# Kernel tuning notes

Measured on AMD Instinct MI355X. Metric: run time of the kernel, lower is better.

Reference implementation:

```python
import jax, jax.numpy as jnp
import numpy as np

H = 128
G = 8192            # num session graphs
TOTAL = 409600      # total nodes across all graphs
MAX_ITEM = 10000


def setup_inputs() -> dict:
    key = jax.random.key(0)
    ks = jax.random.split(key, 16)
    rng = np.random.default_rng(0)
    # variable-length sections that sum exactly to TOTAL
    secs = rng.integers(10, 90, size=G - 1)
    last = TOTAL - int(secs.sum())
    assert last >= 1
    sections = np.concatenate([secs, [last]]).astype(np.int32)
    segment_ids = np.repeat(np.arange(G, dtype=np.int32), sections)
    last_idx = (np.cumsum(sections) - 1).astype(np.int32)

    s = 0.02
    inp = {
        "node_embedding": jax.random.normal(ks[0], (TOTAL, H), jnp.float32),
        "num_count": jax.random.uniform(ks[1], (TOTAL,), jnp.float32),
        "sections": jnp.asarray(sections),
        "segment_ids": jnp.asarray(segment_ids),
        "last_idx": jnp.asarray(last_idx),
        "item_embedding_table": jax.random.normal(ks[2], (MAX_ITEM, H), jnp.float32),
        "user_embedding": jax.random.normal(ks[3], (G, H), jnp.float32),
        "u_n_repeat": jnp.zeros((G, H), jnp.float32),
        "max_item_id": MAX_ITEM,
        "W1_w": jax.random.normal(ks[4], (H, H), jnp.float32) * s,
        "W1_b": jnp.zeros((H,), jnp.float32),
        "W2_w": jax.random.normal(ks[5], (H, H), jnp.float32) * s,
        "W2_b": jnp.zeros((H,), jnp.float32),
        "q_w": jax.random.normal(ks[6], (1, H), jnp.float32) * s,
        "q_b": jnp.zeros((1,), jnp.float32),
        "W3_w": jax.random.normal(ks[7], (H, 2 * H), jnp.float32) * s,
        "W3_b": jnp.zeros((H,), jnp.float32),
    }
    return inp


def reference(node_embedding, num_count, sections, segment_ids, last_idx,
              item_embedding_table, user_embedding, u_n_repeat, max_item_id,
              W1_w, W1_b, W2_w, W2_b, q_w, q_b, W3_w, W3_b):
    num_graphs = last_idx.shape[0]
    # last node of each graph, [G, H]
    v_n = node_embedding[last_idx]
    # broadcast last node back to every node of its graph (replaces torch.split repeat loop)
    v_n_rep = v_n[segment_ids]                          # [N, H]
    gate = jax.nn.sigmoid(v_n_rep @ W1_w.T + W1_b + node_embedding @ W2_w.T + W2_b)
    alpha = gate @ q_w.T + q_b                          # [N, 1]
    s_g_whole = num_count[:, None] * alpha * node_embedding  # [N, H]
    s_g = jax.ops.segment_sum(s_g_whole, segment_ids, num_segments=num_graphs)  # [G, H]
    s_h = jnp.concatenate([v_n, s_g], axis=1) @ W3_w.T + W3_b  # [G, H]
    return s_h
```

## Files before the change

### kernel.cpp

```cpp
#include <hip/hip_runtime.h>
#include <hip/hip_bf16.h>

#define H_DIM  128
#define NGRAPH 8192
#define NTOTAL 409600
#define NBLK2  (NTOTAL / 128)

#define NLOG2E -1.4426950408889634f

typedef __attribute__((ext_vector_type(8))) short    s16x8;
typedef __attribute__((ext_vector_type(4))) float    f32x4;
typedef __attribute__((ext_vector_type(4))) unsigned u32x4;

__device__ __forceinline__ unsigned short f2bf(float f) {
    unsigned int u = __float_as_uint(f);
    unsigned int r = u + 0x7fffu + ((u >> 16) & 1u);
    return (unsigned short)(r >> 16);
}

__global__ void k0_w2(const float* __restrict__ W2w, unsigned short* __restrict__ w2bf) {
    int i = blockIdx.x * 256 + threadIdx.x;
    w2bf[i] = f2bf(NLOG2E * W2w[i]);
}

__global__ __launch_bounds__(128) void k1_ag(
    const float* __restrict__ node_emb,
    const int*   __restrict__ last_idx,
    const float* __restrict__ W1w,
    const float* __restrict__ W1b,
    const float* __restrict__ W2b,
    float* __restrict__ a_g,
    float* __restrict__ s_g)
{
    __shared__ float vn[4][H_DIM];
    const int tid = threadIdx.x;
    const int g0  = blockIdx.x * 4;
    #pragma unroll
    for (int g = 0; g < 4; g++) {
        int li = last_idx[g0 + g];
        vn[g][tid] = node_emb[(size_t)li * H_DIM + tid];
        s_g[(size_t)(g0 + g) * H_DIM + tid] = 0.f;
    }
    __syncthreads();
    float b = W1b[tid] + W2b[tid];
    float a0 = b, a1 = b, a2 = b, a3 = b;
    const float* wrow = W1w + (size_t)tid * H_DIM;
    #pragma unroll 8
    for (int k = 0; k < H_DIM; k += 4) {
        float4 w = *reinterpret_cast<const float4*>(wrow + k);
        a0 += w.x * vn[0][k] + w.y * vn[0][k+1] + w.z * vn[0][k+2] + w.w * vn[0][k+3];
        a1 += w.x * vn[1][k] + w.y * vn[1][k+1] + w.z * vn[1][k+2] + w.w * vn[1][k+3];
        a2 += w.x * vn[2][k] + w.y * vn[2][k+1] + w.z * vn[2][k+2] + w.w * vn[2][k+3];
        a3 += w.x * vn[3][k] + w.y * vn[3][k+1] + w.z * vn[3][k+2] + w.w * vn[3][k+3];
    }
    a_g[(size_t)(g0 + 0) * H_DIM + tid] = NLOG2E * a0;
    a_g[(size_t)(g0 + 1) * H_DIM + tid] = NLOG2E * a1;
    a_g[(size_t)(g0 + 2) * H_DIM + tid] = NLOG2E * a2;
    a_g[(size_t)(g0 + 3) * H_DIM + tid] = NLOG2E * a3;
}

__global__ __launch_bounds__(512, 6) void k2_fused(
    const float* __restrict__ node_emb,
    const float* __restrict__ num_count,
    const int*   __restrict__ seg_ids,
    const float* __restrict__ a_g,
    const unsigned short* __restrict__ w2bf,
    const float* __restrict__ q_w,
    const float* __restrict__ q_b,
    float* __restrict__ s_g)
{
    __shared__ __align__(16) char w2s[H_DIM * 256];

    const int tid = threadIdx.x;
    {
        const uint4* wsrc = reinterpret_cast<const uint4*>(w2bf);
        #pragma unroll
        for (int i = 0; i < 4; i++) {
            int c = i * 512 + tid;
            uint4 v = wsrc[c];
            int byte = c << 4;
            int row  = byte >> 8;
            *reinterpret_cast<uint4*>(w2s + (byte ^ ((row & 7) << 4))) = v;
        }
    }

    const int bid = (int)blockIdx.x;
    const int swz = (bid & 7) * (NBLK2 / 8) + (bid >> 3);

    const int lane = tid & 63;
    const int wid  = tid >> 6;
    const int l16 = lane & 15, lq = lane >> 4;
    const int nb  = (swz * 8 + wid) * 16;

    const int   sgl = seg_ids[nb + l16];
    const float ncl = num_count[nb + l16];
    const float qb0 = q_b[0];

    const float* agrow = a_g + (size_t)sgl * H_DIM + lq * 4;
    f32x4 acc[8];
    #pragma unroll
    for (int nt = 0; nt < 8; nt++) {
        float4 a4 = *reinterpret_cast<const float4*>(agrow + nt * 16);
        acc[nt] = f32x4{a4.x, a4.y, a4.z, a4.w};
    }

    s16x8 af[4];
    const float* nrow = node_emb + (size_t)(nb + l16) * H_DIM + lq * 8;
    #pragma unroll
    for (int ks = 0; ks < 4; ks++) {
        float4 f0 = *reinterpret_cast<const float4*>(nrow + ks * 32);
        float4 f1 = *reinterpret_cast<const float4*>(nrow + ks * 32 + 4);
        unsigned p0, p1, p2, p3;
        asm("v_cvt_pk_bf16_f32 %0, %1, %2" : "=v"(p0) : "v"(f0.x), "v"(f0.y));
        asm("v_cvt_pk_bf16_f32 %0, %1, %2" : "=v"(p1) : "v"(f0.z), "v"(f0.w));
        asm("v_cvt_pk_bf16_f32 %0, %1, %2" : "=v"(p2) : "v"(f1.x), "v"(f1.y));
        asm("v_cvt_pk_bf16_f32 %0, %1, %2" : "=v"(p3) : "v"(f1.z), "v"(f1.w));
        union { u32x4 u; s16x8 s; } cv;
        cv.u = u32x4{p0, p1, p2, p3};
        af[ks] = cv.s;
    }

    __syncthreads();

    #pragma unroll
    for (int ks = 0; ks < 4; ks++) {
        #pragma unroll
        for (int nt = 0; nt < 8; nt++) {
            int row  = nt * 16 + l16;
            int byte = (row << 8) | ((lq * 8 + ks * 32) << 1);
            byte ^= (row & 7) << 4;
            s16x8 wfr = *reinterpret_cast<const s16x8*>(w2s + byte);
            acc[nt] = __builtin_amdgcn_mfma_f32_16x16x32_bf16(wfr, af[ks], acc[nt], 0, 0, 0);
        }
    }

    float pp0 = 0.f, pp1 = 0.f, pp2 = 0.f, pp3 = 0.f;
    #pragma unroll
    for (int nt = 0; nt < 8; nt++) {
        float4 q4 = *reinterpret_cast<const float4*>(q_w + nt * 16 + lq * 4);
        pp0 += q4.x * __builtin_amdgcn_rcpf(1.f + __builtin_amdgcn_exp2f(acc[nt][0]));
        pp1 += q4.y * __builtin_amdgcn_rcpf(1.f + __builtin_amdgcn_exp2f(acc[nt][1]));
        pp2 += q4.z * __builtin_amdgcn_rcpf(1.f + __builtin_amdgcn_exp2f(acc[nt][2]));
        pp3 += q4.w * __builtin_amdgcn_rcpf(1.f + __builtin_amdgcn_exp2f(acc[nt][3]));
    }
    float p = (pp0 + pp1) + (pp2 + pp3);
    p += __shfl_xor(p, 16, 64);
    p += __shfl_xor(p, 32, 64);
    const float coefl = ncl * (p + qb0);

    s16x8 ib[2];
    #pragma unroll
    for (int b = 0; b < 2; b++) {
        int kk = l16 + 16 * b;
        #pragma unroll
        for (int e = 0; e < 8; e++)
            ib[b][e] = (kk == lq * 8 + e) ? (short)0x3F80 : (short)0;
    }
    f32x4 accT[4][2];
    #pragma unroll
    for (int ks = 0; ks < 4; ks++)
        #pragma unroll
        for (int b = 0; b < 2; b++)
            accT[ks][b] = __builtin_amdgcn_mfma_f32_16x16x32_bf16(
                              af[ks], ib[b], f32x4{0.f, 0.f, 0.f, 0.f}, 0, 0, 0);

    int r0 = 0;
    while (r0 < 16) {
        const int cur = __shfl(sgl, r0, 64);
        unsigned long long diff = __ballot(sgl != cur) & 0xFFFFull;
        diff &= ~((1ull << r0) - 1ull);
        const int r1 = diff ? (int)__builtin_ctzll(diff) : 16;

        const float cmask = (sgl == cur) ? coefl : 0.f;
        float cm[4];
        #pragma unroll
        for (int rr = 0; rr < 4; rr++)
            cm[rr] = __shfl(cmask, lq * 4 + rr, 64);

        #pragma unroll
        for (int ks = 0; ks < 4; ks++) {
            #pragma unroll
            for (int b = 0; b < 2; b++) {
                float s = cm[0] * accT[ks][b][0] + cm[1] * accT[ks][b][1]
                        + cm[2] * accT[ks][b][2] + cm[3] * accT[ks][b][3];
                s += __shfl_xor(s, 16, 64);
                s += __shfl_xor(s, 32, 64);
                if (lq == 0)
                    atomicAdd(s_g + (size_t)cur * H_DIM + ks * 32 + b * 16 + l16, s);
            }
        }
        r0 = r1;
    }
}

__global__ __launch_bounds__(128) void k3_out(
    const float* __restrict__ node_emb,
    const int*   __restrict__ last_idx,
    const float* __restrict__ s_g,
    const float* __restrict__ W3w,
    const float* __restrict__ W3b,
    float* __restrict__ out)
{
    __shared__ float cat[8][2 * H_DIM];
    const int tid = threadIdx.x;
    const int g0  = blockIdx.x * 8;
    #pragma unroll
    for (int g = 0; g < 8; g++) {
        cat[g][tid]         = node_emb[(size_t)last_idx[g0 + g] * H_DIM + tid];
        cat[g][H_DIM + tid] = s_g[(size_t)(g0 + g) * H_DIM + tid];
    }
    __syncthreads();
    float acc[8];
    float b = W3b[tid];
    #pragma unroll
    for (int g = 0; g < 8; g++) acc[g] = b;
    const float* wrow = W3w + (size_t)tid * (2 * H_DIM);
    for (int k = 0; k < 2 * H_DIM; k += 4) {
        float4 w = *reinterpret_cast<const float4*>(wrow + k);
        #pragma unroll
        for (int g = 0; g < 8; g++)
            acc[g] += w.x * cat[g][k] + w.y * cat[g][k+1]
                    + w.z * cat[g][k+2] + w.w * cat[g][k+3];
    }
    #pragma unroll
    for (int g = 0; g < 8; g++)
        out[(size_t)(g0 + g) * H_DIM + tid] = acc[g];
}

extern "C" void kernel_launch(void* const* d_in, const int* in_sizes, int n_in,
                              void* d_out, int out_size, void* d_ws, size_t ws_size,
                              hipStream_t stream) {
    const float* node_emb  = (const float*)d_in[0];
    const float* num_count = (const float*)d_in[1];
    const int*   seg_ids   = (const int*)d_in[3];
    const int*   last_idx  = (const int*)d_in[4];
    const float* W1w = (const float*)d_in[9];
    const float* W1b = (const float*)d_in[10];
    const float* W2w = (const float*)d_in[11];
    const float* W2b = (const float*)d_in[12];
    const float* qw  = (const float*)d_in[13];
    const float* qb  = (const float*)d_in[14];
    const float* W3w = (const float*)d_in[15];
    const float* W3b = (const float*)d_in[16];
    float* out = (float*)d_out;

    char* ws = (char*)d_ws;
    float* a_g = (float*)(ws);
    float* s_g = (float*)(ws + (4u << 20));
    unsigned short* w2bf = (unsigned short*)(ws + (8u << 20));

    k0_w2   <<<64,         256, 0, stream>>>(W2w, w2bf);
    k1_ag   <<<NGRAPH / 4, 128, 0, stream>>>(node_emb, last_idx, W1w, W1b, W2b, a_g, s_g);
    k2_fused<<<NBLK2,      512, 0, stream>>>(node_emb, num_count, seg_ids, a_g,
                                             w2bf, qw, qb, s_g);
    k3_out  <<<NGRAPH / 8, 128, 0, stream>>>(node_emb, last_idx, s_g, W3w, W3b, out);
}
```

Measured before the change: 107.2 us.

## Reduce segment sums in LDS per block and merge boundary partials in a gather kernel

Global atomicAdd into s_g is replaced by LDS atomics into a per-block table of up to 14 local graphs. After a sync, each block writes interior graphs straight to s_g and writes the partial sums of its first and last boundary graphs to a part buffer. A new gather kernel adds up the partials for graphs that span blocks, so s_g no longer needs zeroing in k1. The occupancy hint rises from 6 to 8 blocks per CU. This trades global atomic traffic for an extra launch, about 7 KB more LDS per block, and the assumption that no 128-node block touches more than 14 graphs.

```diff
diff --git a/kernel.cpp b/kernel.cpp
--- a/kernel.cpp
+++ b/kernel.cpp
@@ -5,6 +5,7 @@
 #define NGRAPH 8192
 #define NTOTAL 409600
 #define NBLK2  (NTOTAL / 128)
+#define MAXLOC 14
 
 #define NLOG2E -1.4426950408889634f
 
@@ -29,8 +30,7 @@
     const float* __restrict__ W1w,
     const float* __restrict__ W1b,
     const float* __restrict__ W2b,
-    float* __restrict__ a_g,
-    float* __restrict__ s_g)
+    float* __restrict__ a_g)
 {
     __shared__ float vn[4][H_DIM];
     const int tid = threadIdx.x;
@@ -39,7 +39,6 @@
     for (int g = 0; g < 4; g++) {
         int li = last_idx[g0 + g];
         vn[g][tid] = node_emb[(size_t)li * H_DIM + tid];
-        s_g[(size_t)(g0 + g) * H_DIM + tid] = 0.f;
     }
     __syncthreads();
     float b = W1b[tid] + W2b[tid];
@@ -59,20 +58,26 @@
     a_g[(size_t)(g0 + 3) * H_DIM + tid] = NLOG2E * a3;
 }
 
-__global__ __launch_bounds__(512, 6) void k2_fused(
+__global__ __launch_bounds__(512, 8) void k2_fused(
     const float* __restrict__ node_emb,
     const float* __restrict__ num_count,
     const int*   __restrict__ seg_ids,
+    const int*   __restrict__ last_idx,
     const float* __restrict__ a_g,
     const unsigned short* __restrict__ w2bf,
     const float* __restrict__ q_w,
     const float* __restrict__ q_b,
-    float* __restrict__ s_g)
+    float* __restrict__ s_g,
+    float* __restrict__ part)
 {
     __shared__ __align__(16) char w2s[H_DIM * 256];
+    __shared__ float ldsS[MAXLOC][H_DIM];
 
     const int tid = threadIdx.x;
     {
+        float* z = &ldsS[0][0];
+        #pragma unroll
+        for (int i = tid; i < MAXLOC * H_DIM; i += 512) z[i] = 0.f;
         const uint4* wsrc = reinterpret_cast<const uint4*>(w2bf);
         #pragma unroll
         for (int i = 0; i < 4; i++) {
@@ -90,8 +95,10 @@
     const int lane = tid & 63;
     const int wid  = tid >> 6;
     const int l16 = lane & 15, lq = lane >> 4;
-    const int nb  = (swz * 8 + wid) * 16;
-
+    const int nbB = swz * 128;
+    const int nb  = nbB + wid * 16;
+
+    const int   sg0 = seg_ids[nbB];
     const int   sgl = seg_ids[nb + l16];
     const float ncl = num_count[nb + l16];
     const float qb0 = q_b[0];
@@ -177,20 +184,57 @@
         for (int rr = 0; rr < 4; rr++)
             cm[rr] = __shfl(cmask, lq * 4 + rr, 64);
 
+        const int loc = cur - sg0;
         #pragma unroll
         for (int ks = 0; ks < 4; ks++) {
             #pragma unroll
             for (int b = 0; b < 2; b++) {
                 float s = cm[0] * accT[ks][b][0] + cm[1] * accT[ks][b][1]
                         + cm[2] * accT[ks][b][2] + cm[3] * accT[ks][b][3];
-                s += __shfl_xor(s, 16, 64);
-                s += __shfl_xor(s, 32, 64);
-                if (lq == 0)
-                    atomicAdd(s_g + (size_t)cur * H_DIM + ks * 32 + b * 16 + l16, s);
+                atomicAdd(&ldsS[loc][ks * 32 + b * 16 + l16], s);
             }
         }
         r0 = r1;
     }
+    __syncthreads();
+
+    {
+        const int sgL  = seg_ids[nbB + 127];
+        const int nloc = sgL - sg0 + 1;
+        const int col  = tid & 127;
+        for (int j = tid >> 7; j < nloc; j += 4) {
+            const int gg = sg0 + j;
+            const int st = gg ? (last_idx[gg - 1] + 1) : 0;
+            const int en = last_idx[gg];
+            const float v = ldsS[j][col];
+            const bool interior = (st >= nbB) && (en < nbB + 128);
+            if (interior) {
+                s_g[(size_t)gg * H_DIM + col] = v;
+            } else if (j == 0) {
+                part[((size_t)swz * 2 + 0) * H_DIM + col] = v;
+            } else {
+                part[((size_t)swz * 2 + 1) * H_DIM + col] = v;
+            }
+        }
+    }
+}
+
+__global__ __launch_bounds__(128) void k2b_gather(
+    const int*   __restrict__ last_idx,
+    const float* __restrict__ part,
+    float* __restrict__ s_g)
+{
+    const int g   = blockIdx.x;
+    const int col = threadIdx.x;
+    const int st  = g ? (last_idx[g - 1] + 1) : 0;
+    const int en  = last_idx[g];
+    const int bs  = st >> 7, be = en >> 7;
+    if (bs == be) return;
+    const int slot0 = (st == (bs << 7)) ? 0 : 1;
+    float s = part[((size_t)bs * 2 + slot0) * H_DIM + col];
+    for (int m = bs + 1; m <= be; m++)
+        s += part[((size_t)m * 2 + 0) * H_DIM + col];
+    s_g[(size_t)g * H_DIM + col] = s;
 }
 
 __global__ __launch_bounds__(128) void k3_out(
@@ -245,13 +289,15 @@
     float* out = (float*)d_out;
 
     char* ws = (char*)d_ws;
-    float* a_g = (float*)(ws);
-    float* s_g = (float*)(ws + (4u << 20));
+    float* a_g  = (float*)(ws);
+    float* s_g  = (float*)(ws + (4u << 20));
     unsigned short* w2bf = (unsigned short*)(ws + (8u << 20));
-
-    k0_w2   <<<64,         256, 0, stream>>>(W2w, w2bf);
-    k1_ag   <<<NGRAPH / 4, 128, 0, stream>>>(node_emb, last_idx, W1w, W1b, W2b, a_g, s_g);
-    k2_fused<<<NBLK2,      512, 0, stream>>>(node_emb, num_count, seg_ids, a_g,
-                                             w2bf, qw, qb, s_g);
-    k3_out  <<<NGRAPH / 8, 128, 0, stream>>>(node_emb, last_idx, s_g, W3w, W3b, out);
-}
+    float* part = (float*)(ws + (9u << 20));
+
+    k0_w2     <<<64,         256, 0, stream>>>(W2w, w2bf);
+    k1_ag     <<<NGRAPH / 4, 128, 0, stream>>>(node_emb, last_idx, W1w, W1b, W2b, a_g);
+    k2_fused  <<<NBLK2,      512, 0, stream>>>(node_emb, num_count, seg_ids, last_idx,
+                                               a_g, w2bf, qw, qb, s_g, part);
+    k2b_gather<<<NGRAPH,     128, 0, stream>>>(last_idx, part, s_g);
+    k3_out    <<<NGRAPH / 8, 128, 0, stream>>>(node_emb, last_idx, s_g, W3w, W3b, out);
+}
```

Measured after the change: 185.1 us. 1.73x slower.

## Convert W1 and W3 to bf16 and compute per-graph gate projection with MFMA

Applied to the files above, without the earlier changes.

A single prep kernel now converts W1, W2 and W3 to bf16 and precomputes the summed bias. The W1·v_n projection kernel is rewritten to stage W1 in swizzled LDS and run 16x16x32 bf16 MFMA over 128 graphs per block, replacing the scalar fp32 FMA loop. The output kernel reads W3 as bf16 to halve its weight traffic. The intent is to cut the cost of the small per-graph GEMMs, which were scalar and bandwidth-heavy, at the price of lower precision on v_n and the W1/W3 weights.

```diff
diff --git a/kernel.cpp b/kernel.cpp
--- a/kernel.cpp
+++ b/kernel.cpp
@@ -18,45 +18,102 @@
     return (unsigned short)(r >> 16);
 }
 
-__global__ void k0_w2(const float* __restrict__ W2w, unsigned short* __restrict__ w2bf) {
+__global__ __launch_bounds__(256) void k0_prep(
+    const float* __restrict__ W1w, const float* __restrict__ W2w,
+    const float* __restrict__ W3w, const float* __restrict__ W1b,
+    const float* __restrict__ W2b,
+    unsigned short* __restrict__ w1bf, unsigned short* __restrict__ w2bf,
+    unsigned short* __restrict__ w3bf, float* __restrict__ bsum)
+{
     int i = blockIdx.x * 256 + threadIdx.x;
-    w2bf[i] = f2bf(NLOG2E * W2w[i]);
-}
-
-__global__ __launch_bounds__(128) void k1_ag(
+    if (i < 16384)      w1bf[i] = f2bf(W1w[i]);
+    else if (i < 32768) w2bf[i - 16384] = f2bf(NLOG2E * W2w[i - 16384]);
+    else                w3bf[i - 32768] = f2bf(W3w[i - 32768]);
+    if (i < H_DIM) bsum[i] = W1b[i] + W2b[i];
+}
+
+__global__ __launch_bounds__(512) void k1_ag(
     const float* __restrict__ node_emb,
     const int*   __restrict__ last_idx,
-    const float* __restrict__ W1w,
-    const float* __restrict__ W1b,
-    const float* __restrict__ W2b,
+    const unsigned short* __restrict__ w1bf,
+    const float* __restrict__ bsum,
     float* __restrict__ a_g,
     float* __restrict__ s_g)
 {
-    __shared__ float vn[4][H_DIM];
+    __shared__ __align__(16) char w1s[H_DIM * 256];
+
     const int tid = threadIdx.x;
-    const int g0  = blockIdx.x * 4;
-    #pragma unroll
-    for (int g = 0; g < 4; g++) {
-        int li = last_idx[g0 + g];
-        vn[g][tid] = node_emb[(size_t)li * H_DIM + tid];
-        s_g[(size_t)(g0 + g) * H_DIM + tid] = 0.f;
-    }
+    {
+        const uint4* wsrc = reinterpret_cast<const uint4*>(w1bf);
+        #pragma unroll
+        for (int i = 0; i < 4; i++) {
+            int c = i * 512 + tid;
+            uint4 v = wsrc[c];
+            int byte = c << 4;
+            int row  = byte >> 8;
+            *reinterpret_cast<uint4*>(w1s + (byte ^ ((row & 7) << 4))) = v;
+        }
+    }
+    {
+        float4* z = reinterpret_cast<float4*>(s_g + (size_t)blockIdx.x * 128 * H_DIM);
+        float4 zero = float4{0.f, 0.f, 0.f, 0.f};
+        #pragma unroll
+        for (int i = 0; i < 8; i++) z[i * 512 + tid] = zero;
+    }
+
+    const int lane = tid & 63;
+    const int wid  = tid >> 6;
+    const int l16 = lane & 15, lq = lane >> 4;
+    const int g   = blockIdx.x * 128 + wid * 16 + l16;
+    const int li  = last_idx[g];
+
+    f32x4 acc[8];
+    #pragma unroll
+    for (int nt = 0; nt < 8; nt++) {
+        float4 b4 = *reinterpret_cast<const float4*>(bsum + nt * 16 + lq * 4);
+        acc[nt] = f32x4{b4.x, b4.y, b4.z, b4.w};
+    }
+
+    s16x8 vf[4];
+    const float* vnrow = node_emb + (size_t)li * H_DIM + lq * 8;
+    #pragma unroll
+    for (int ks = 0; ks < 4; ks++) {
+        float4 f0 = *reinterpret_cast<const float4*>(vnrow + ks * 32);
+        float4 f1 = *reinterpret_cast<const float4*>(vnrow + ks * 32 + 4);
+        unsigned p0, p1, p2, p3;
+        asm("v_cvt_pk_bf16_f32 %0, %1, %2" : "=v"(p0) : "v"(f0.x), "v"(f0.y));
+        asm("v_cvt_pk_bf16_f32 %0, %1, %2" : "=v"(p1) : "v"(f0.z), "v"(f0.w));
+        asm("v_cvt_pk_bf16_f32 %0, %1, %2" : "=v"(p2) : "v"(f1.x), "v"(f1.y));
+        asm("v_cvt_pk_bf16_f32 %0, %1, %2" : "=v"(p3) : "v"(f1.z), "v"(f1.w));
+        union { u32x4 u; s16x8 s; } cv;
+        cv.u = u32x4{p0, p1, p2, p3};
+        vf[ks] = cv.s;
+    }
+
     __syncthreads();
-    float b = W1b[tid] + W2b[tid];
-    float a0 = b, a1 = b, a2 = b, a3 = b;
-    const float* wrow = W1w + (size_t)tid * H_DIM;
-    #pragma unroll 8
-    for (int k = 0; k < H_DIM; k += 4) {
-        float4 w = *reinterpret_cast<const float4*>(wrow + k);
-        a0 += w.x * vn[0][k] + w.y * vn[0][k+1] + w.z * vn[0][k+2] + w.w * vn[0][k+3];
-        a1 += w.x * vn[1][k] + w.y * vn[1][k+1] + w.z * vn[1][k+2] + w.w * vn[1][k+3];
-        a2 += w.x * vn[2][k] + w.y * vn[2][k+1] + w.z * vn[2][k+2] + w.w * vn[2][k+3];
-        a3 += w.x * vn[3][k] + w.y * vn[3][k+1] + w.z * vn[3][k+2] + w.w * vn[3][k+3];
-    }
-    a_g[(size_t)(g0 + 0) * H_DIM + tid] = NLOG2E * a0;
-    a_g[(size_t)(g0 + 1) * H_DIM + tid] = NLOG2E * a1;
-    a_g[(size_t)(g0 + 2) * H_DIM + tid] = NLOG2E * a2;
-    a_g[(size_t)(g0 + 3) * H_DIM + tid] = NLOG2E * a3;
+
+    #pragma unroll
+    for (int ks = 0; ks < 4; ks++) {
+        #pragma unroll
+        for (int nt = 0; nt < 8; nt++) {
+            int row  = nt * 16 + l16;
+            int byte = (row << 8) | ((lq * 8 + ks * 32) << 1);
+            byte ^= (row & 7) << 4;
+            s16x8 wfr = *reinterpret_cast<const s16x8*>(w1s + byte);
+            acc[nt] = __builtin_amdgcn_mfma_f32_16x16x32_bf16(wfr, vf[ks], acc[nt], 0, 0, 0);
+        }
+    }
+
+    float* arow = a_g + (size_t)g * H_DIM + lq * 4;
+    #pragma unroll
+    for (int nt = 0; nt < 8; nt++) {
+        float4 o;
+        o.x = NLOG2E * acc[nt][0];
+        o.y = NLOG2E * acc[nt][1];
+        o.z = NLOG2E * acc[nt][2];
+        o.w = NLOG2E * acc[nt][3];
+        *reinterpret_cast<float4*>(arow + nt * 16) = o;
+    }
 }
 
 __global__ __launch_bounds__(512, 6) void k2_fused(
@@ -197,7 +254,7 @@
     const float* __restrict__ node_emb,
     const int*   __restrict__ last_idx,
     const float* __restrict__ s_g,
-    const float* __restrict__ W3w,
+    const unsigned short* __restrict__ w3bf,
     const float* __restrict__ W3b,
     float* __restrict__ out)
 {
@@ -214,13 +271,17 @@
     float b = W3b[tid];
     #pragma unroll
     for (int g = 0; g < 8; g++) acc[g] = b;
-    const float* wrow = W3w + (size_t)tid * (2 * H_DIM);
+    const uint2* wrow = reinterpret_cast<const uint2*>(w3bf + (size_t)tid * (2 * H_DIM));
     for (int k = 0; k < 2 * H_DIM; k += 4) {
-        float4 w = *reinterpret_cast<const float4*>(wrow + k);
+        uint2 w = wrow[k >> 2];
+        float w0 = __uint_as_float(w.x << 16);
+        float w1 = __uint_as_float(w.x & 0xffff0000u);
+        float w2 = __uint_as_float(w.y << 16);
+        float w3 = __uint_as_float(w.y & 0xffff0000u);
         #pragma unroll
         for (int g = 0; g < 8; g++)
-            acc[g] += w.x * cat[g][k] + w.y * cat[g][k+1]
-                    + w.z * cat[g][k+2] + w.w * cat[g][k+3];
+            acc[g] += w0 * cat[g][k] + w1 * cat[g][k+1]
+                    + w2 * cat[g][k+2] + w3 * cat[g][k+3];
     }
     #pragma unroll
     for (int g = 0; g < 8; g++)
@@ -248,10 +309,14 @@
     float* a_g = (float*)(ws);
     float* s_g = (float*)(ws + (4u << 20));
     unsigned short* w2bf = (unsigned short*)(ws + (8u << 20));
-
-    k0_w2   <<<64,         256, 0, stream>>>(W2w, w2bf);
-    k1_ag   <<<NGRAPH / 4, 128, 0, stream>>>(node_emb, last_idx, W1w, W1b, W2b, a_g, s_g);
-    k2_fused<<<NBLK2,      512, 0, stream>>>(node_emb, num_count, seg_ids, a_g,
-                                             w2bf, qw, qb, s_g);
-    k3_out  <<<NGRAPH / 8, 128, 0, stream>>>(node_emb, last_idx, s_g, W3w, W3b, out);
-}
+    unsigned short* w1bf = (unsigned short*)(ws + (8u << 20) + 32768);
+    unsigned short* w3bf = (unsigned short*)(ws + (8u << 20) + 65536);
+    float* bsum          = (float*)(ws + (8u << 20) + 131072);
+
+    k0_prep<<<256,        256, 0, stream>>>(W1w, W2w, W3w, W1b, W2b,
+                                            w1bf, w2bf, w3bf, bsum);
+    k1_ag  <<<NGRAPH/128, 512, 0, stream>>>(node_emb, last_idx, w1bf, bsum, a_g, s_g);
+    k2_fused<<<NBLK2,     512, 0, stream>>>(node_emb, num_count, seg_ids, a_g,
+                                            w2bf, qw, qb, s_g);
+    k3_out <<<NGRAPH/8,   128, 0, stream>>>(node_emb, last_idx, s_g, w3bf, W3b, out);
+}
```

New measurement: 96.38 us (median of 2 runs). 10.1% less time.
